# Performance work log

Hardware: AMD Instinct MI355X
Metric: run time of the kernel (lower is better)

The kernel has to match this reference:

```python
import jax, jax.numpy as jnp
import numpy as np

N = 50000
E = 800000
D_IN = 384
D_H = 128
D_MLP = 128
K = 16


def layer_norm(x, g, b, eps=1e-5):
    m = x.mean(-1, keepdims=True)
    v = ((x - m) ** 2).mean(-1, keepdims=True)
    return (x - m) / jnp.sqrt(v + eps) * g + b


def setup_inputs() -> dict:
    key = jax.random.key(0)
    ks = jax.random.split(key, 16)
    s = lambda d: 1.0 / np.sqrt(d)
    return {
        "x": jax.random.normal(ks[0], (N, D_IN), jnp.float32),
        "edge_index": jax.random.randint(ks[1], (2, E), 0, N, jnp.int64),
        # GCNConv 1
        "W1": jax.random.normal(ks[2], (D_IN, D_H), jnp.float32) * s(D_IN),
        "b1": jnp.zeros((D_H,), jnp.float32),
        "g1": jnp.ones((D_H,), jnp.float32),
        "be1": jnp.zeros((D_H,), jnp.float32),
        # GCNConv 2
        "W2": jax.random.normal(ks[3], (D_H, D_H), jnp.float32) * s(D_H),
        "b2": jnp.zeros((D_H,), jnp.float32),
        "g2": jnp.ones((D_H,), jnp.float32),
        "be2": jnp.zeros((D_H,), jnp.float32),
        # residual projection (input_dim != conv_hidden)
        "rW": jax.random.normal(ks[4], (D_IN, D_H), jnp.float32) * s(D_IN),
        "rb": jnp.zeros((D_H,), jnp.float32),
        "rg": jnp.ones((D_H,), jnp.float32),
        "rbe": jnp.zeros((D_H,), jnp.float32),
        # MLP head
        "mW1": jax.random.normal(ks[5], (D_H, D_MLP), jnp.float32) * s(D_H),
        "mb1": jnp.zeros((D_MLP,), jnp.float32),
        "mg": jnp.ones((D_MLP,), jnp.float32),
        "mbe": jnp.zeros((D_MLP,), jnp.float32),
        "mW2": jax.random.normal(ks[6], (D_MLP, K), jnp.float32) * s(D_MLP),
        "mb2": jnp.zeros((K,), jnp.float32),
    }


def reference(x, edge_index, W1, b1, g1, be1, W2, b2, g2, be2,
              rW, rb, rg, rbe, mW1, mb1, mg, mbe, mW2, mb2):
    n = x.shape[0]
    loops = jnp.arange(n, dtype=edge_index.dtype)
    src = jnp.concatenate([edge_index[0], loops])  # [E+N]
    dst = jnp.concatenate([edge_index[1], loops])
    # symmetric GCN normalization with self-loops
    deg = jax.ops.segment_sum(jnp.ones_like(src, x.dtype), dst, num_segments=n)
    dinv = jnp.where(deg > 0, jax.lax.rsqrt(deg), 0.0)
    norm = dinv[src] * dinv[dst]  # [E+N]

    def gcn_conv(h, W, b):
        hw = h @ W  # [N, D_H]
        msg = hw[src] * norm[:, None]  # gather + scale, [E+N, D_H]
        return jax.ops.segment_sum(msg, dst, num_segments=n) + b

    # layer 1 with projected residual
    h = jax.nn.elu(layer_norm(gcn_conv(x, W1, b1), g1, be1))
    h = h + layer_norm(x @ rW + rb, rg, rbe)
    # layer 2 with identity residual
    h = jax.nn.elu(layer_norm(gcn_conv(h, W2, b2), g2, be2)) + h
    # MLP head (dropout inactive in eval) + softmax over clusters
    z = jax.nn.elu(layer_norm(h @ mW1 + mb1, mg, mbe))
    H = z @ mW2 + mb2
    return jax.nn.softmax(H, axis=1)
```

## Files before the change

kernel.cpp:

```cpp
#include <hip/hip_runtime.h>

#define DH 128

typedef __attribute__((ext_vector_type(8))) short short8;
typedef __attribute__((ext_vector_type(4))) float f32x4;

__device__ __forceinline__ float wave_sum(float v) {
    #pragma unroll
    for (int o = 32; o > 0; o >>= 1) v += __shfl_xor(v, o, 64);
    return v;
}

__device__ __forceinline__ void ln_pair(float v0, float v1, float& o0, float& o1) {
    float m = wave_sum(v0 + v1) * (1.f / 128.f);
    float d0 = v0 - m, d1 = v1 - m;
    float var = wave_sum(d0 * d0 + d1 * d1) * (1.f / 128.f);
    float inv = rsqrtf(var + 1e-5f);
    o0 = d0 * inv; o1 = d1 * inv;
}

__device__ __forceinline__ float elu(float x) { return x > 0.f ? x : expm1f(x); }

__device__ __forceinline__ unsigned short f2bf(float f) {
    unsigned u = __float_as_uint(f);
    u += 0x7fffu + ((u >> 16) & 1u);
    return (unsigned short)(u >> 16);
}
__device__ __forceinline__ float bfl(unsigned u) { return __uint_as_float(u << 16); }
__device__ __forceinline__ float bfh(unsigned u) { return __uint_as_float(u & 0xffff0000u); }
__device__ __forceinline__ unsigned pack_bf2(float a, float b) {
    return (unsigned)f2bf(a) | ((unsigned)f2bf(b) << 16);
}
__device__ __forceinline__ short8 cvt8(float4 v0, float4 v1) {
    short8 o;
    o[0] = (short)f2bf(v0.x); o[1] = (short)f2bf(v0.y);
    o[2] = (short)f2bf(v0.z); o[3] = (short)f2bf(v0.w);
    o[4] = (short)f2bf(v1.x); o[5] = (short)f2bf(v1.y);
    o[6] = (short)f2bf(v1.z); o[7] = (short)f2bf(v1.w);
    return o;
}

__device__ __forceinline__ int xcd_work(int bid, int nwg) {
    int qc = nwg >> 3, rc = nwg & 7;
    int xcd = bid & 7, ix = bid >> 3;
    return (xcd < rc ? xcd * (qc + 1) : rc * (qc + 1) + (xcd - rc) * qc) + ix;
}

__device__ __forceinline__ void lgkm_barrier() {
    asm volatile("s_waitcnt lgkmcnt(0)" ::: "memory");
    __builtin_amdgcn_s_barrier();
    asm volatile("" ::: "memory");
}

__global__ void deg_count_k(const int* __restrict__ dst, int* __restrict__ deg, int E) {
    int e = blockIdx.x * 256 + threadIdx.x;
    if (e < E) atomicAdd(&deg[dst[e]], 1);
}

__global__ __launch_bounds__(1024) void scan_part_k(const int* __restrict__ deg,
                                                    int* __restrict__ rowptr,
                                                    int* __restrict__ bsum,
                                                    float* __restrict__ dinv, int n)
{
    __shared__ int wsum[16];
    const int tid = threadIdx.x, lane = tid & 63, wid = tid >> 6;
    int i = blockIdx.x * 1024 + tid;
    int v = (i < n) ? deg[i] : 0;
    if (i < n) dinv[i] = rsqrtf((float)(v + 1));
    int s = v;
    #pragma unroll
    for (int o = 1; o < 64; o <<= 1) {
        int t = __shfl_up(s, o, 64);
        if (lane >= o) s += t;
    }
    if (lane == 63) wsum[wid] = s;
    __syncthreads();
    if (tid < 16) {
        int ws = wsum[tid];
        #pragma unroll
        for (int o = 1; o < 16; o <<= 1) {
            int t = __shfl_up(ws, o, 64);
            if (tid >= o) ws += t;
        }
        wsum[tid] = ws;
    }
    __syncthreads();
    int excl = (wid ? wsum[wid - 1] : 0) + s - v;
    if (i < n) rowptr[i] = excl;
    if (tid == 0) bsum[blockIdx.x] = wsum[15];
}

__global__ void scan_top_k(int* __restrict__ bsum, int* __restrict__ rowptr_n, int nb) {
    int lane = threadIdx.x;
    int carry = 0;
    for (int base = 0; base < nb; base += 64) {
        int i = base + lane;
        int v = (i < nb) ? bsum[i] : 0;
        int s = v;
        #pragma unroll
        for (int o = 1; o < 64; o <<= 1) {
            int t = __shfl_up(s, o, 64);
            if (lane >= o) s += t;
        }
        if (i < nb) bsum[i] = carry + s - v;
        carry += __shfl(s, 63, 64);
    }
    if (lane == 0) *rowptr_n = carry;
}

__global__ void scan_add_k(const int* __restrict__ bsum, int* __restrict__ rowptr,
                           int* __restrict__ cursor, int n)
{
    int i = blockIdx.x * 256 + threadIdx.x;
    if (i < n) {
        int v = rowptr[i] + bsum[i >> 10];
        rowptr[i] = v;
        cursor[i] = v;
    }
}

__global__ __launch_bounds__(256) void fill_xcd_k(
    const int* __restrict__ src, const int* __restrict__ dst,
    const float* __restrict__ dinv, int* __restrict__ cursor,
    int2* __restrict__ csr, int E, int n)
{
    const int g   = blockIdx.x & 7;
    const int j   = blockIdx.x >> 3;
    const int bpg = gridDim.x >> 3;
    const int per = (n + 7) >> 3;
    const int lo = g * per;
    const int hi = min(n, lo + per);
    for (int e = j * 256 + threadIdx.x; e < E; e += bpg * 256) {
        int d = dst[e];
        if (d >= lo && d < hi) {
            int s = src[e];
            float w = dinv[s] * dinv[d];
            int p = atomicAdd(&cursor[d], 1);
            csr[p] = make_int2(s, __float_as_int(w));
        }
    }
}

__global__ void repack_zero_k(const float* __restrict__ W1, const float* __restrict__ rW,
                              const float* __restrict__ W2, const float* __restrict__ mW1,
                              unsigned short* __restrict__ Wp, int* __restrict__ deg, int n)
{
    int idx = blockIdx.x * 256 + threadIdx.x;
    if (idx < n) deg[idx] = 0;
    if (idx >= 131072) return;
    const float* W; int base;
    if (idx < 49152)       { W = W1;  base = 0; }
    else if (idx < 98304)  { W = rW;  base = 49152; }
    else if (idx < 114688) { W = W2;  base = 98304; }
    else                   { W = mW1; base = 114688; }
    int l = idx - base;
    int kb = l >> 12, rem = l & 4095;
    int nn = rem >> 5, ki = rem & 31;
    Wp[idx] = f2bf(W[(kb * 32 + ki) * DH + nn]);
}

__global__ __launch_bounds__(256, 2) void gemm1_k(
    const float* __restrict__ Af,
    const unsigned short* __restrict__ Bp1, const unsigned short* __restrict__ Bp2,
    const float* __restrict__ bb,
    unsigned short* __restrict__ outa, unsigned short* __restrict__ outb, int n)
{
    constexpr int K = 384, NT = 6;
    __shared__ __align__(16) unsigned short smem[24576];
    unsigned short* smB = smem + 16384;

    const int tid = threadIdx.x;
    const int wid = tid >> 6, lane = tid & 63;
    const int m16 = lane & 15, q = lane >> 4;

    const int work = xcd_work(blockIdx.x, gridDim.x);
    const int rblk = work >> 2;
    const int var  = work & 3;
    const int mat = var >> 1;
    const int c0  = (var & 1) * 64;
    const unsigned short* Bp = mat ? Bp2 : Bp1;
    unsigned short* outp = mat ? outb : outa;
    const float* bias = mat ? bb : nullptr;
    const long long rowbase = (long long)rblk * 128;

    const float* pA[4];
    unsigned short* dA[4];
    #pragma unroll
    for (int u = 0; u < 4; ++u) {
        int j = tid + 256 * u;
        int r = j >> 3, c = j & 7;
        long long gr = rowbase + r; if (gr > (long long)n - 1) gr = n - 1;
        pA[u] = Af + gr * K + c * 8;
        dA[u] = smem + r * 64 + ((c ^ (r & 7)) * 8);
    }
    const unsigned short* pB[2];
    unsigned short* dB[2];
    #pragma unroll
    for (int v = 0; v < 2; ++v) {
        int j = tid + 256 * v;
        int cl = j >> 3, c = j & 7;
        pB[v] = Bp + (c >> 2) * 4096 + (c0 + cl) * 32 + (c & 3) * 8;
        dB[v] = smB + cl * 64 + ((c ^ (cl & 7)) * 8);
    }

    float4 raf[2][4][2];
    short8 rbv[2][2];

    auto loadT = [&](int t, int buf) {
        #pragma unroll
        for (int u = 0; u < 4; ++u) {
            raf[buf][u][0] = *(const float4*)(pA[u] + t * 64);
            raf[buf][u][1] = *(const float4*)(pA[u] + t * 64 + 4);
        }
        #pragma unroll
        for (int v = 0; v < 2; ++v)
            rbv[buf][v] = *(const short8*)(pB[v] + t * 8192);
    };
    auto writeT = [&](int buf) {
        #pragma unroll
        for (int u = 0; u < 4; ++u)
            *(short8*)(dA[u] + buf * 8192) = cvt8(raf[buf][u][0], raf[buf][u][1]);
        #pragma unroll
        for (int v = 0; v < 2; ++v)
            *(short8*)(dB[v] + buf * 4096) = rbv[buf][v];
    };

    f32x4 acc[2][4];
    const f32x4 zero = {0.f, 0.f, 0.f, 0.f};
    #pragma unroll
    for (int mi = 0; mi < 2; ++mi)
        #pragma unroll
        for (int nj = 0; nj < 4; ++nj) acc[mi][nj] = zero;

    int sC[2];
    #pragma unroll
    for (int ks = 0; ks < 2; ++ks) sC[ks] = (((ks * 4 + q) ^ (m16 & 7)) * 8);
    const int arow = wid * 32 + m16;

    loadT(0, 0);
    loadT(1, 1);
    writeT(0);
    lgkm_barrier();

    #pragma unroll
    for (int t = 0; t < NT; ++t) {
        const int buf = t & 1;
        const unsigned short* a0 = smem + buf * 8192;
        const unsigned short* b0 = smB + buf * 4096;
        short8 af[2][2], bf[2][4];
        #pragma unroll
        for (int ks = 0; ks < 2; ++ks) {
            af[ks][0] = *(const short8*)(a0 + arow * 64 + sC[ks]);
            af[ks][1] = *(const short8*)(a0 + (arow + 16) * 64 + sC[ks]);
            #pragma unroll
            for (int nj = 0; nj < 4; ++nj)
                bf[ks][nj] = *(const short8*)(b0 + (nj * 16 + m16) * 64 + sC[ks]);
        }
        if (t + 2 < NT) loadT(t + 2, buf);
        if (t + 1 < NT) writeT(buf ^ 1);
        #pragma unroll
        for (int ks = 0; ks < 2; ++ks)
            #pragma unroll
            for (int nj = 0; nj < 4; ++nj) {
                acc[0][nj] = __builtin_amdgcn_mfma_f32_16x16x32_bf16(af[ks][0], bf[ks][nj], acc[0][nj], 0, 0, 0);
                acc[1][nj] = __builtin_amdgcn_mfma_f32_16x16x32_bf16(af[ks][1], bf[ks][nj], acc[1][nj], 0, 0, 0);
            }
        lgkm_barrier();
    }

    #pragma unroll
    for (int nj = 0; nj < 4; ++nj) {
        int cl = nj * 16 + m16;
        float bv = bias ? bias[c0 + cl] : 0.f;
        #pragma unroll
        for (int mi = 0; mi < 2; ++mi)
            #pragma unroll
            for (int r = 0; r < 4; ++r)
                smem[(wid * 32 + mi * 16 + q * 4 + r) * 72 + cl] = f2bf(acc[mi][nj][r] + bv);
    }
    __syncthreads();
    #pragma unroll
    for (int h = 0; h < 4; ++h) {
        int idx = tid + h * 256;
        int row = idx >> 3, c8 = idx & 7;
        long long grow = rowbase + row;
        if (grow < n)
            *(short8*)(outp + grow * DH + c0 + c8 * 8) = *(const short8*)(smem + row * 72 + c8 * 8);
    }
}

__global__ __launch_bounds__(256, 3) void gemm_k128(
    const unsigned short* __restrict__ A,
    const unsigned short* __restrict__ Bp, const float* __restrict__ bias,
    unsigned short* __restrict__ outp, int n)
{
    __shared__ __align__(16) unsigned short smem[24576];
    unsigned short* smB = smem + 16384;

    const int tid = threadIdx.x;
    const int wid = tid >> 6, lane = tid & 63;
    const int m16 = lane & 15, q = lane >> 4;

    const int work = xcd_work(blockIdx.x, gridDim.x);
    const int rblk = work >> 1;
    const int c0 = (work & 1) * 64;
    const long long rowbase = (long long)rblk * 128;

    #pragma unroll
    for (int r = 0; r < 8; ++r) {
        int j = r * 256 + tid;
        int row = j >> 4, c16 = j & 15;
        long long grow = rowbase + row; if (grow > (long long)n - 1) grow = n - 1;
        *(short8*)(smem + row * 128 + ((c16 ^ (row & 15)) * 8)) =
            *(const short8*)(A + grow * 128 + c16 * 8);
    }
    #pragma unroll
    for (int r = 0; r < 4; ++r) {
        int j = r * 256 + tid;
        int kb = j >> 8, rem = j & 255;
        int cl = rem >> 2, qq = rem & 3;
        *(short8*)(smB + kb * 2048 + qq * 512 + cl * 8) =
            *(const short8*)(Bp + kb * 4096 + c0 * 32 + rem * 8);
    }
    __syncthreads();

    f32x4 acc[2][4];
    const f32x4 zero = {0.f, 0.f, 0.f, 0.f};
    #pragma unroll
    for (int mi = 0; mi < 2; ++mi)
        #pragma unroll
        for (int nj = 0; nj < 4; ++nj) acc[mi][nj] = zero;

    const int frow = wid * 32 + m16;
    #pragma unroll
    for (int kb = 0; kb < 4; ++kb) {
        short8 af0 = *(const short8*)(smem + frow * 128 + (((kb * 4 + q) ^ m16) * 8));
        short8 af1 = *(const short8*)(smem + (frow + 16) * 128 + (((kb * 4 + q) ^ m16) * 8));
        #pragma unroll
        for (int nj = 0; nj < 4; ++nj) {
            short8 bf = *(const short8*)(smB + kb * 2048 + q * 512 + (nj * 16 + m16) * 8);
            acc[0][nj] = __builtin_amdgcn_mfma_f32_16x16x32_bf16(af0, bf, acc[0][nj], 0, 0, 0);
            acc[1][nj] = __builtin_amdgcn_mfma_f32_16x16x32_bf16(af1, bf, acc[1][nj], 0, 0, 0);
        }
    }

    __syncthreads();
    #pragma unroll
    for (int nj = 0; nj < 4; ++nj) {
        int cl = nj * 16 + m16;
        float bv = bias ? bias[c0 + cl] : 0.f;
        #pragma unroll
        for (int mi = 0; mi < 2; ++mi)
            #pragma unroll
            for (int r = 0; r < 4; ++r)
                smem[(wid * 32 + mi * 16 + q * 4 + r) * 72 + cl] = f2bf(acc[mi][nj][r] + bv);
    }
    __syncthreads();
    #pragma unroll
    for (int h = 0; h < 4; ++h) {
        int idx = tid + h * 256;
        int row = idx >> 3, c8 = idx & 7;
        long long grow = rowbase + row;
        if (grow < n)
            *(short8*)(outp + grow * DH + c0 + c8 * 8) = *(const short8*)(smem + row * 72 + c8 * 8);
    }
}

__device__ __forceinline__ void gather_row(
    const unsigned* __restrict__ hw, const int2* __restrict__ csr,
    int beg, int end, int lane, float& o0, float& o1)
{
    beg = __builtin_amdgcn_readfirstlane(beg);
    end = __builtin_amdgcn_readfirstlane(end);
    float a0 = 0.f, a1 = 0.f, b0 = 0.f, b1 = 0.f;
    float c0 = 0.f, c1 = 0.f, d0 = 0.f, d1 = 0.f;
    int p = beg;
    for (; p + 15 < end; p += 16) {
        int2 e[16];
        #pragma unroll
        for (int i = 0; i < 16; ++i) e[i] = csr[p + i];
        unsigned u[16];
        #pragma unroll
        for (int i = 0; i < 16; ++i) u[i] = hw[(long long)e[i].x * 64 + lane];
        #pragma unroll
        for (int i = 0; i < 16; ++i) {
            float w = __int_as_float(e[i].y);
            float lo = bfl(u[i]), hi = bfh(u[i]);
            if ((i & 3) == 0)      { a0 = fmaf(w, lo, a0); a1 = fmaf(w, hi, a1); }
            else if ((i & 3) == 1) { b0 = fmaf(w, lo, b0); b1 = fmaf(w, hi, b1); }
            else if ((i & 3) == 2) { c0 = fmaf(w, lo, c0); c1 = fmaf(w, hi, c1); }
            else                   { d0 = fmaf(w, lo, d0); d1 = fmaf(w, hi, d1); }
        }
    }
    for (; p + 3 < end; p += 4) {
        int2 e0 = csr[p], e1 = csr[p + 1], e2 = csr[p + 2], e3 = csr[p + 3];
        unsigned u0 = hw[(long long)e0.x * 64 + lane];
        unsigned u1 = hw[(long long)e1.x * 64 + lane];
        unsigned u2 = hw[(long long)e2.x * 64 + lane];
        unsigned u3 = hw[(long long)e3.x * 64 + lane];
        float w0 = __int_as_float(e0.y), w1 = __int_as_float(e1.y);
        float w2 = __int_as_float(e2.y), w3 = __int_as_float(e3.y);
        a0 = fmaf(w0, bfl(u0), a0);  a1 = fmaf(w0, bfh(u0), a1);
        b0 = fmaf(w1, bfl(u1), b0);  b1 = fmaf(w1, bfh(u1), b1);
        c0 = fmaf(w2, bfl(u2), c0);  c1 = fmaf(w2, bfh(u2), c1);
        d0 = fmaf(w3, bfl(u3), d0);  d1 = fmaf(w3, bfh(u3), d1);
    }
    for (; p < end; ++p) {
        int2 e0 = csr[p];
        unsigned u0 = hw[(long long)e0.x * 64 + lane];
        float w0 = __int_as_float(e0.y);
        a0 = fmaf(w0, bfl(u0), a0);
        a1 = fmaf(w0, bfh(u0), a1);
    }
    o0 = (a0 + b0) + (c0 + d0);
    o1 = (a1 + b1) + (c1 + d1);
}

__global__ __launch_bounds__(256) void gfuse1_k(
    const unsigned* __restrict__ hw, const unsigned* __restrict__ proj,
    const int* __restrict__ rowptr, const int2* __restrict__ csr,
    const float* __restrict__ dinv,
    const float* __restrict__ b1, const float* __restrict__ g1, const float* __restrict__ be1,
    const float* __restrict__ rg, const float* __restrict__ rbe,
    unsigned* __restrict__ hout, int n)
{
    int row = blockIdx.x * 4 + (threadIdx.x >> 6);
    if (row >= n) return;
    int lane = threadIdx.x & 63;
    float a0, a1;
    gather_row(hw, csr, rowptr[row], rowptr[row + 1], lane, a0, a1);
    long long off = (long long)row * 64;
    float di = dinv[row], sl = di * di;
    unsigned us = hw[off + lane];
    float2 bv  = *(const float2*)(b1 + 2 * lane);
    float2 gv  = *(const float2*)(g1 + 2 * lane);
    float2 bev = *(const float2*)(be1 + 2 * lane);
    float2 rgv = *(const float2*)(rg + 2 * lane);
    float2 rbv = *(const float2*)(rbe + 2 * lane);
    float v0 = a0 + sl * bfl(us) + bv.x;
    float v1 = a1 + sl * bfh(us) + bv.y;
    float o0, o1; ln_pair(v0, v1, o0, o1);
    float t0 = elu(o0 * gv.x + bev.x);
    float t1 = elu(o1 * gv.y + bev.y);
    unsigned up = proj[off + lane];
    float q0, q1; ln_pair(bfl(up), bfh(up), q0, q1);
    hout[off + lane] = pack_bf2(t0 + q0 * rgv.x + rbv.x, t1 + q1 * rgv.y + rbv.y);
}

__global__ __launch_bounds__(256) void gfuse2_k(
    const unsigned* __restrict__ hw, const unsigned* __restrict__ hprev,
    const int* __restrict__ rowptr, const int2* __restrict__ csr,
    const float* __restrict__ dinv,
    const float* __restrict__ b2, const float* __restrict__ g2, const float* __restrict__ be2,
    unsigned* __restrict__ h2, int n)
{
    int row = blockIdx.x * 4 + (threadIdx.x >> 6);
    if (row >= n) return;
    int lane = threadIdx.x & 63;
    float a0, a1;
    gather_row(hw, csr, rowptr[row], rowptr[row + 1], lane, a0, a1);
    long long off = (long long)row * 64;
    float di = dinv[row], sl = di * di;
    unsigned us = hw[off + lane];
    float2 bv  = *(const float2*)(b2 + 2 * lane);
    float2 gv  = *(const float2*)(g2 + 2 * lane);
    float2 bev = *(const float2*)(be2 + 2 * lane);
    float v0 = a0 + sl * bfl(us) + bv.x;
    float v1 = a1 + sl * bfh(us) + bv.y;
    float o0, o1; ln_pair(v0, v1, o0, o1);
    float t0 = elu(o0 * gv.x + bev.x);
    float t1 = elu(o1 * gv.y + bev.y);
    unsigned uh = hprev[off + lane];
    h2[off + lane] = pack_bf2(t0 + bfl(uh), t1 + bfh(uh));
}

__global__ __launch_bounds__(256) void head_k(
    const unsigned* __restrict__ zraw, const float* __restrict__ g, const float* __restrict__ be,
    const float* __restrict__ mW2, const float* __restrict__ mb2,
    float* __restrict__ out, int n)
{
    int row = blockIdx.x * 4 + (threadIdx.x >> 6);
    if (row >= n) return;
    int lane = threadIdx.x & 63;
    unsigned u = zraw[(long long)row * 64 + lane];
    float o0, o1; ln_pair(bfl(u), bfh(u), o0, o1);
    float2 gv  = *(const float2*)(g + 2 * lane);
    float2 bev = *(const float2*)(be + 2 * lane);
    float z0 = elu(o0 * gv.x + bev.x);
    float z1 = elu(o1 * gv.y + bev.y);
    int k = lane & 15, seg = lane >> 4;
    float acc = 0.f;
    #pragma unroll
    for (int t = 0; t < 16; ++t) {
        int srcl = seg * 16 + t;
        float zz0 = __shfl(z0, srcl, 64);
        float zz1 = __shfl(z1, srcl, 64);
        int c = seg * 32 + 2 * t;
        acc = fmaf(zz0, mW2[c * 16 + k], acc);
        acc = fmaf(zz1, mW2[(c + 1) * 16 + k], acc);
    }
    acc += __shfl_xor(acc, 32, 64);
    acc += __shfl_xor(acc, 16, 64);
    float hk = acc + mb2[k];
    float mx = hk;
    #pragma unroll
    for (int o = 8; o > 0; o >>= 1) mx = fmaxf(mx, __shfl_xor(mx, o, 64));
    float e = expf(hk - mx);
    float s = e;
    #pragma unroll
    for (int o = 8; o > 0; o >>= 1) s += __shfl_xor(s, o, 64);
    if (lane < 16) out[(long long)row * 16 + k] = e / s;
}

static inline size_t align16(size_t x) { return (x + 15) & ~(size_t)15; }

extern "C" void kernel_launch(void* const* d_in, const int* in_sizes, int n_in,
                              void* d_out, int out_size, void* d_ws, size_t ws_size,
                              hipStream_t stream)
{
    const float* x   = (const float*)d_in[0];
    const int*   ei  = (const int*)d_in[1];
    const float* W1  = (const float*)d_in[2];
    const float* b1  = (const float*)d_in[3];
    const float* g1  = (const float*)d_in[4];
    const float* be1 = (const float*)d_in[5];
    const float* W2  = (const float*)d_in[6];
    const float* b2  = (const float*)d_in[7];
    const float* g2  = (const float*)d_in[8];
    const float* be2 = (const float*)d_in[9];
    const float* rW  = (const float*)d_in[10];
    const float* rb  = (const float*)d_in[11];
    const float* rg  = (const float*)d_in[12];
    const float* rbe = (const float*)d_in[13];
    const float* mW1 = (const float*)d_in[14];
    const float* mb1 = (const float*)d_in[15];
    const float* mg  = (const float*)d_in[16];
    const float* mbe = (const float*)d_in[17];
    const float* mW2 = (const float*)d_in[18];
    const float* mb2 = (const float*)d_in[19];
    float* out = (float*)d_out;

    const int n = in_sizes[0] / 384;
    const int E = in_sizes[1] / 2;
    const int* src = ei;
    const int* dst = ei + E;

    char* w = (char*)d_ws;
    int* deg     = (int*)w;   w += align16((size_t)n * 4);
    int* rowptr  = (int*)w;   w += align16((size_t)(n + 1) * 4);
    int* cursor  = (int*)w;   w += align16((size_t)n * 4);
    float* dinv  = (float*)w; w += align16((size_t)n * 4);
    int* bsum    = (int*)w;   w += align16((size_t)1024 * 4);
    int2* csr    = (int2*)w;  w += align16((size_t)E * 8);
    unsigned short* hw1  = (unsigned short*)w; w += align16((size_t)n * DH * 2);
    unsigned short* proj = (unsigned short*)w; w += align16((size_t)n * DH * 2);
    unsigned short* hbuf = (unsigned short*)w; w += align16((size_t)n * DH * 2);
    unsigned short* Wp   = (unsigned short*)w; w += align16((size_t)131072 * 2);
    unsigned short* Wp1 = Wp;
    unsigned short* Wpr = Wp + 49152;
    unsigned short* Wp2 = Wp + 98304;
    unsigned short* WpM = Wp + 114688;
    unsigned short* hw2  = hw1;
    unsigned short* h2   = proj;
    unsigned short* zraw = hbuf;

    int gE = (E + 255) / 256;
    int gN = (n + 255) / 256;
    int nb = (n + 1023) / 1024;
    int rblks = (n + 127) / 128;
    int gRow4 = (n + 3) / 4;

    repack_zero_k<<<512, 256, 0, stream>>>(W1, rW, W2, mW1, Wp, deg, n);

    deg_count_k<<<gE, 256, 0, stream>>>(dst, deg, E);
    scan_part_k<<<nb, 1024, 0, stream>>>(deg, rowptr, bsum, dinv, n);
    scan_top_k<<<1, 64, 0, stream>>>(bsum, rowptr + n, nb);
    scan_add_k<<<gN, 256, 0, stream>>>(bsum, rowptr, cursor, n);
    fill_xcd_k<<<1024, 256, 0, stream>>>(src, dst, dinv, cursor, csr, E, n);

    gemm1_k<<<rblks * 4, 256, 0, stream>>>(x, Wp1, Wpr, rb, hw1, proj, n);
    gfuse1_k<<<gRow4, 256, 0, stream>>>((unsigned*)hw1, (unsigned*)proj, rowptr, csr, dinv,
                                        b1, g1, be1, rg, rbe, (unsigned*)hbuf, n);

    gemm_k128<<<rblks * 2, 256, 0, stream>>>(hbuf, Wp2, nullptr, hw2, n);
    gfuse2_k<<<gRow4, 256, 0, stream>>>((unsigned*)hw2, (unsigned*)hbuf, rowptr, csr, dinv,
                                        b2, g2, be2, (unsigned*)h2, n);

    gemm_k128<<<rblks * 2, 256, 0, stream>>>(h2, WpM, mb1, zraw, n);
    head_k<<<gRow4, 256, 0, stream>>>((unsigned*)zraw, mg, mbe, mW2, mb2, out, n);
}
```

Before: 400.9 us.

## Pre-convert x to bf16 and stream GEMM1 tiles via direct global-to-LDS loads

Adds a kernel that converts x to bf16 once. GEMM1 now reads the bf16 copy and fills its A and B tiles with global_load_lds, which writes straight into LDS and skips the register staging and per-iteration conversion. The swizzle moves into the global address, and occupancy is raised to 3 waves per SIMD. The cost is an extra pass over x: a 77MB fp32 read plus a 38MB bf16 write. GEMM1 previously read x in fp32 four times, once per column variant, so this trade may or may not pay off.

```diff
diff --git a/kernel.cpp b/kernel.cpp
--- a/kernel.cpp
+++ b/kernel.cpp
@@ -46,10 +46,23 @@
     return (xcd < rc ? xcd * (qc + 1) : rc * (qc + 1) + (xcd - rc) * qc) + ix;
 }
 
-__device__ __forceinline__ void lgkm_barrier() {
-    asm volatile("s_waitcnt lgkmcnt(0)" ::: "memory");
-    __builtin_amdgcn_s_barrier();
-    asm volatile("" ::: "memory");
+__device__ __forceinline__ void gload_lds16(const unsigned short* gp, unsigned short* lp) {
+    __builtin_amdgcn_global_load_lds(
+        (const __attribute__((address_space(1))) void*)gp,
+        (__attribute__((address_space(3))) void*)lp, 16, 0, 0);
+}
+
+__global__ __launch_bounds__(256) void conv_x_k(const float* __restrict__ x,
+                                                unsigned short* __restrict__ xb,
+                                                long long n8)
+{
+    long long i = (long long)blockIdx.x * 256 + threadIdx.x;
+    long long stride = (long long)gridDim.x * 256;
+    for (; i < n8; i += stride) {
+        float4 v0 = *(const float4*)(x + i * 8);
+        float4 v1 = *(const float4*)(x + i * 8 + 4);
+        *(short8*)(xb + i * 8) = cvt8(v0, v1);
+    }
 }
 
 __global__ void deg_count_k(const int* __restrict__ dst, int* __restrict__ deg, int E) {
@@ -159,13 +172,13 @@
     Wp[idx] = f2bf(W[(kb * 32 + ki) * DH + nn]);
 }
 
-__global__ __launch_bounds__(256, 2) void gemm1_k(
-    const float* __restrict__ Af,
+__global__ __launch_bounds__(256, 3) void gemm1_k(
+    const unsigned short* __restrict__ xb,
     const unsigned short* __restrict__ Bp1, const unsigned short* __restrict__ Bp2,
     const float* __restrict__ bb,
     unsigned short* __restrict__ outa, unsigned short* __restrict__ outb, int n)
 {
-    constexpr int K = 384, NT = 6;
+    constexpr int NT = 6;
     __shared__ __align__(16) unsigned short smem[24576];
     unsigned short* smB = smem + 16384;
 
@@ -183,46 +196,36 @@
     const float* bias = mat ? bb : nullptr;
     const long long rowbase = (long long)rblk * 128;
 
-    const float* pA[4];
-    unsigned short* dA[4];
-    #pragma unroll
-    for (int u = 0; u < 4; ++u) {
-        int j = tid + 256 * u;
-        int r = j >> 3, c = j & 7;
+    const unsigned short* gA[4];
+    int ldsA[4];
+    #pragma unroll
+    for (int i = 0; i < 4; ++i) {
+        int j = wid * 4 + i;
+        int r = j * 8 + (lane >> 3);
+        int c = lane & 7;
         long long gr = rowbase + r; if (gr > (long long)n - 1) gr = n - 1;
-        pA[u] = Af + gr * K + c * 8;
-        dA[u] = smem + r * 64 + ((c ^ (r & 7)) * 8);
-    }
-    const unsigned short* pB[2];
-    unsigned short* dB[2];
-    #pragma unroll
-    for (int v = 0; v < 2; ++v) {
-        int j = tid + 256 * v;
-        int cl = j >> 3, c = j & 7;
-        pB[v] = Bp + (c >> 2) * 4096 + (c0 + cl) * 32 + (c & 3) * 8;
-        dB[v] = smB + cl * 64 + ((c ^ (cl & 7)) * 8);
-    }
-
-    float4 raf[2][4][2];
-    short8 rbv[2][2];
-
-    auto loadT = [&](int t, int buf) {
-        #pragma unroll
-        for (int u = 0; u < 4; ++u) {
-            raf[buf][u][0] = *(const float4*)(pA[u] + t * 64);
-            raf[buf][u][1] = *(const float4*)(pA[u] + t * 64 + 4);
-        }
-        #pragma unroll
-        for (int v = 0; v < 2; ++v)
-            rbv[buf][v] = *(const short8*)(pB[v] + t * 8192);
-    };
-    auto writeT = [&](int buf) {
-        #pragma unroll
-        for (int u = 0; u < 4; ++u)
-            *(short8*)(dA[u] + buf * 8192) = cvt8(raf[buf][u][0], raf[buf][u][1]);
-        #pragma unroll
-        for (int v = 0; v < 2; ++v)
-            *(short8*)(dB[v] + buf * 4096) = rbv[buf][v];
+        gA[i] = xb + gr * 384 + ((c ^ (r & 7)) * 8);
+        ldsA[i] = j * 512;
+    }
+    const unsigned short* gB[2];
+    int ldsB[2];
+    #pragma unroll
+    for (int i = 0; i < 2; ++i) {
+        int j2 = wid * 2 + i;
+        int cl = j2 * 8 + (lane >> 3);
+        int c = lane & 7;
+        int cp = c ^ (cl & 7);
+        gB[i] = Bp + (cp >> 2) * 4096 + (c0 + cl) * 32 + (cp & 3) * 8;
+        ldsB[i] = j2 * 512;
+    }
+
+    auto issueT = [&](int t, int buf) {
+        #pragma unroll
+        for (int i = 0; i < 4; ++i)
+            gload_lds16(gA[i] + t * 64, smem + buf * 8192 + ldsA[i]);
+        #pragma unroll
+        for (int i = 0; i < 2; ++i)
+            gload_lds16(gB[i] + t * 8192, smB + buf * 4096 + ldsB[i]);
     };
 
     f32x4 acc[2][4];
@@ -232,32 +235,28 @@
         #pragma unroll
         for (int nj = 0; nj < 4; ++nj) acc[mi][nj] = zero;
 
-    int sC[2];
-    #pragma unroll
-    for (int ks = 0; ks < 2; ++ks) sC[ks] = (((ks * 4 + q) ^ (m16 & 7)) * 8);
     const int arow = wid * 32 + m16;
-
-    loadT(0, 0);
-    loadT(1, 1);
-    writeT(0);
-    lgkm_barrier();
+    const int s8a = m16 & 7;
+
+    issueT(0, 0);
+    __syncthreads();
 
     #pragma unroll
     for (int t = 0; t < NT; ++t) {
         const int buf = t & 1;
+        if (t + 1 < NT) issueT(t + 1, buf ^ 1);
         const unsigned short* a0 = smem + buf * 8192;
         const unsigned short* b0 = smB + buf * 4096;
         short8 af[2][2], bf[2][4];
         #pragma unroll
         for (int ks = 0; ks < 2; ++ks) {
-            af[ks][0] = *(const short8*)(a0 + arow * 64 + sC[ks]);
-            af[ks][1] = *(const short8*)(a0 + (arow + 16) * 64 + sC[ks]);
+            int co = ((ks * 4 + q) ^ s8a) * 8;
+            af[ks][0] = *(const short8*)(a0 + arow * 64 + co);
+            af[ks][1] = *(const short8*)(a0 + (arow + 16) * 64 + co);
             #pragma unroll
             for (int nj = 0; nj < 4; ++nj)
-                bf[ks][nj] = *(const short8*)(b0 + (nj * 16 + m16) * 64 + sC[ks]);
+                bf[ks][nj] = *(const short8*)(b0 + (nj * 16 + m16) * 64 + co);
         }
-        if (t + 2 < NT) loadT(t + 2, buf);
-        if (t + 1 < NT) writeT(buf ^ 1);
         #pragma unroll
         for (int ks = 0; ks < 2; ++ks)
             #pragma unroll
@@ -265,7 +264,7 @@
                 acc[0][nj] = __builtin_amdgcn_mfma_f32_16x16x32_bf16(af[ks][0], bf[ks][nj], acc[0][nj], 0, 0, 0);
                 acc[1][nj] = __builtin_amdgcn_mfma_f32_16x16x32_bf16(af[ks][1], bf[ks][nj], acc[1][nj], 0, 0, 0);
             }
-        lgkm_barrier();
+        __syncthreads();
     }
 
     #pragma unroll
@@ -552,6 +551,7 @@
     float* dinv  = (float*)w; w += align16((size_t)n * 4);
     int* bsum    = (int*)w;   w += align16((size_t)1024 * 4);
     int2* csr    = (int2*)w;  w += align16((size_t)E * 8);
+    unsigned short* xb   = (unsigned short*)w; w += align16((size_t)n * 384 * 2);
     unsigned short* hw1  = (unsigned short*)w; w += align16((size_t)n * DH * 2);
     unsigned short* proj = (unsigned short*)w; w += align16((size_t)n * DH * 2);
     unsigned short* hbuf = (unsigned short*)w; w += align16((size_t)n * DH * 2);
@@ -570,6 +570,7 @@
     int rblks = (n + 127) / 128;
     int gRow4 = (n + 3) / 4;
 
+    conv_x_k<<<2048, 256, 0, stream>>>(x, xb, (long long)n * 48);
     repack_zero_k<<<512, 256, 0, stream>>>(W1, rW, W2, mW1, Wp, deg, n);
 
     deg_count_k<<<gE, 256, 0, stream>>>(dst, deg, E);
@@ -578,7 +579,7 @@
     scan_add_k<<<gN, 256, 0, stream>>>(bsum, rowptr, cursor, n);
     fill_xcd_k<<<1024, 256, 0, stream>>>(src, dst, dinv, cursor, csr, E, n);
 
-    gemm1_k<<<rblks * 4, 256, 0, stream>>>(x, Wp1, Wpr, rb, hw1, proj, n);
+    gemm1_k<<<rblks * 4, 256, 0, stream>>>(xb, Wp1, Wpr, rb, hw1, proj, n);
     gfuse1_k<<<gRow4, 256, 0, stream>>>((unsigned*)hw1, (unsigned*)proj, rowptr, csr, dinv,
                                         b1, g1, be1, rg, rbe, (unsigned*)hbuf, n);
 
```

Measured after the change: 402.3 us. Within noise of the previous version (+0.3%).

## Fuse MLP head GEMM with layernorm, ELU, projection and softmax

Applied to the files above, without the earlier changes.

Replaces the separate 128x128 GEMM (which wrote bf16 zraw to global memory) and the per-row head kernel with one kernel. Each block computes a 128-row tile of h2 @ mW1 with MFMA, stages it in LDS, then runs layernorm, ELU, the 128x16 projection and softmax per row from LDS. This removes one launch and a full N x 128 bf16 write and read. In exchange, each block uses 64KB of LDS and every wave loops serially over 32 rows, which may lower occupancy and parallelism.

```diff
diff --git a/kernel.cpp b/kernel.cpp
--- a/kernel.cpp
+++ b/kernel.cpp
@@ -363,6 +363,104 @@
         long long grow = rowbase + row;
         if (grow < n)
             *(short8*)(outp + grow * DH + c0 + c8 * 8) = *(const short8*)(smem + row * 72 + c8 * 8);
+    }
+}
+
+__global__ __launch_bounds__(256, 2) void mlp_head_k(
+    const unsigned short* __restrict__ A,
+    const unsigned short* __restrict__ Bp,
+    const float* __restrict__ mb1,
+    const float* __restrict__ mg, const float* __restrict__ mbe,
+    const float* __restrict__ mW2, const float* __restrict__ mb2,
+    float* __restrict__ out, int n)
+{
+    __shared__ __align__(16) unsigned short smem[32768];
+    unsigned short* smB = smem + 16384;
+
+    const int tid = threadIdx.x;
+    const int wid = tid >> 6, lane = tid & 63;
+    const int m16 = lane & 15, q = lane >> 4;
+    const long long rowbase = (long long)blockIdx.x * 128;
+
+    #pragma unroll
+    for (int r = 0; r < 8; ++r) {
+        int j = r * 256 + tid;
+        int row = j >> 4, c16 = j & 15;
+        long long grow = rowbase + row; if (grow > (long long)n - 1) grow = n - 1;
+        *(short8*)(smem + row * 128 + ((c16 ^ (row & 15)) * 8)) =
+            *(const short8*)(A + grow * 128 + c16 * 8);
+    }
+    #pragma unroll
+    for (int r = 0; r < 8; ++r) {
+        int j = r * 256 + tid;
+        *(short8*)(smB + j * 8) = *(const short8*)(Bp + j * 8);
+    }
+    __syncthreads();
+
+    f32x4 acc[2][8];
+    const f32x4 zero = {0.f, 0.f, 0.f, 0.f};
+    #pragma unroll
+    for (int mi = 0; mi < 2; ++mi)
+        #pragma unroll
+        for (int nj = 0; nj < 8; ++nj) acc[mi][nj] = zero;
+
+    const int frow = wid * 32 + m16;
+    #pragma unroll
+    for (int kb = 0; kb < 4; ++kb) {
+        short8 af0 = *(const short8*)(smem + frow * 128 + (((kb * 4 + q) ^ m16) * 8));
+        short8 af1 = *(const short8*)(smem + (frow + 16) * 128 + (((kb * 4 + q) ^ m16) * 8));
+        #pragma unroll
+        for (int nj = 0; nj < 8; ++nj) {
+            short8 bf = *(const short8*)(smB + kb * 4096 + (nj * 16 + m16) * 32 + q * 8);
+            acc[0][nj] = __builtin_amdgcn_mfma_f32_16x16x32_bf16(af0, bf, acc[0][nj], 0, 0, 0);
+            acc[1][nj] = __builtin_amdgcn_mfma_f32_16x16x32_bf16(af1, bf, acc[1][nj], 0, 0, 0);
+        }
+    }
+
+    __syncthreads();
+    #pragma unroll
+    for (int nj = 0; nj < 8; ++nj) {
+        int col = nj * 16 + m16;
+        float b = mb1[col];
+        #pragma unroll
+        for (int mi = 0; mi < 2; ++mi)
+            #pragma unroll
+            for (int r = 0; r < 4; ++r)
+                smem[(wid * 32 + mi * 16 + q * 4 + r) * 136 + col] = f2bf(acc[mi][nj][r] + b);
+    }
+    __syncthreads();
+
+    const int k = lane & 15, seg = lane >> 4;
+    for (int rr = 0; rr < 32; ++rr) {
+        int row = wid * 32 + rr;
+        long long grow = rowbase + row;
+        unsigned u = *(const unsigned*)(smem + row * 136 + 2 * lane);
+        float o0, o1; ln_pair(bfl(u), bfh(u), o0, o1);
+        float2 gv  = *(const float2*)(mg + 2 * lane);
+        float2 bev = *(const float2*)(mbe + 2 * lane);
+        float z0 = elu(o0 * gv.x + bev.x);
+        float z1 = elu(o1 * gv.y + bev.y);
+        float acch = 0.f;
+        #pragma unroll
+        for (int t = 0; t < 16; ++t) {
+            int srcl = seg * 16 + t;
+            float zz0 = __shfl(z0, srcl, 64);
+            float zz1 = __shfl(z1, srcl, 64);
+            int c = seg * 32 + 2 * t;
+            acch = fmaf(zz0, mW2[c * 16 + k], acch);
+            acch = fmaf(zz1, mW2[(c + 1) * 16 + k], acch);
+        }
+        acch += __shfl_xor(acch, 32, 64);
+        acch += __shfl_xor(acch, 16, 64);
+        float hk = acch + mb2[k];
+        float mx = hk;
+        #pragma unroll
+        for (int o = 8; o > 0; o >>= 1) mx = fmaxf(mx, __shfl_xor(mx, o, 64));
+        float e = expf(hk - mx);
+        float s = e;
+        #pragma unroll
+        for (int o = 8; o > 0; o >>= 1) s += __shfl_xor(s, o, 64);
+        if (lane < 16 && grow < n) out[grow * 16 + k] = e / s;
     }
 }
 
@@ -474,44 +572,6 @@
     h2[off + lane] = pack_bf2(t0 + bfl(uh), t1 + bfh(uh));
 }
 
-__global__ __launch_bounds__(256) void head_k(
-    const unsigned* __restrict__ zraw, const float* __restrict__ g, const float* __restrict__ be,
-    const float* __restrict__ mW2, const float* __restrict__ mb2,
-    float* __restrict__ out, int n)
-{
-    int row = blockIdx.x * 4 + (threadIdx.x >> 6);
-    if (row >= n) return;
-    int lane = threadIdx.x & 63;
-    unsigned u = zraw[(long long)row * 64 + lane];
-    float o0, o1; ln_pair(bfl(u), bfh(u), o0, o1);
-    float2 gv  = *(const float2*)(g + 2 * lane);
-    float2 bev = *(const float2*)(be + 2 * lane);
-    float z0 = elu(o0 * gv.x + bev.x);
-    float z1 = elu(o1 * gv.y + bev.y);
-    int k = lane & 15, seg = lane >> 4;
-    float acc = 0.f;
-    #pragma unroll
-    for (int t = 0; t < 16; ++t) {
-        int srcl = seg * 16 + t;
-        float zz0 = __shfl(z0, srcl, 64);
-        float zz1 = __shfl(z1, srcl, 64);
-        int c = seg * 32 + 2 * t;
-        acc = fmaf(zz0, mW2[c * 16 + k], acc);
-        acc = fmaf(zz1, mW2[(c + 1) * 16 + k], acc);
-    }
-    acc += __shfl_xor(acc, 32, 64);
-    acc += __shfl_xor(acc, 16, 64);
-    float hk = acc + mb2[k];
-    float mx = hk;
-    #pragma unroll
-    for (int o = 8; o > 0; o >>= 1) mx = fmaxf(mx, __shfl_xor(mx, o, 64));
-    float e = expf(hk - mx);
-    float s = e;
-    #pragma unroll
-    for (int o = 8; o > 0; o >>= 1) s += __shfl_xor(s, o, 64);
-    if (lane < 16) out[(long long)row * 16 + k] = e / s;
-}
-
 static inline size_t align16(size_t x) { return (x + 15) & ~(size_t)15; }
 
 extern "C" void kernel_launch(void* const* d_in, const int* in_sizes, int n_in,
@@ -562,7 +622,6 @@
     unsigned short* WpM = Wp + 114688;
     unsigned short* hw2  = hw1;
     unsigned short* h2   = proj;
-    unsigned short* zraw = hbuf;
 
     int gE = (E + 255) / 256;
     int gN = (n + 255) / 256;
@@ -586,6 +645,5 @@
     gfuse2_k<<<gRow4, 256, 0, stream>>>((unsigned*)hw2, (unsigned*)hbuf, rowptr, csr, dinv,
                                         b2, g2, be2, (unsigned*)h2, n);
 
-    gemm_k128<<<rblks * 2, 256, 0, stream>>>(h2, WpM, mb1, zraw, n);
-    head_k<<<gRow4, 256, 0, stream>>>((unsigned*)zraw, mg, mbe, mW2, mb2, out, n);
-}
+    mlp_head_k<<<rblks, 256, 0, stream>>>(h2, WpM, mb1, mg, mbe, mW2, mb2, out, n);
+}
```

New measurement: 415.9 us. +3.7%, slower.
